# Performance work log

Hardware: AMD Instinct MI355X
Metric: run time of the kernel (lower is better)

## Reference

```python
import jax, jax.numpy as jnp
import numpy as np

ALPHA = 0.12
BETA = 0.88
OMEGA = 6.0
PHI_BASE = 0.0
B, T, D = 4, 4096, 2048


def setup_inputs() -> dict:
    key = jax.random.key(0)
    k1, = jax.random.split(key, 1)
    x = jax.random.normal(k1, (B, T, D), dtype=jnp.float32)
    gate = jnp.asarray(-2.0, dtype=jnp.float32)          # nn.Parameter gate_init
    input_scale = jnp.asarray(4.0, dtype=jnp.float32)     # nn.Parameter init 4.0
    mem_state = jnp.zeros((1, 1, D), dtype=jnp.float32)   # persistent buffer
    return {"x": x, "gate": gate, "input_scale": input_scale,
            "mem_state": mem_state, "step_idx": 0}


def reference(x, gate, input_scale, mem_state, step_idx):
    Bn, Tn, Dn = x.shape
    dtype = x.dtype
    # EMA recurrence: m_t = beta * m_{t-1} + alpha * input_scale * x_t
    u = (ALPHA * input_scale) * x                         # [B,T,D]
    m0 = jnp.broadcast_to(mem_state[:, 0, :], (Bn, Dn))   # [B,D]

    def step(m, u_t):
        m = BETA * m + u_t
        return m, m

    _, ms = jax.lax.scan(step, m0, jnp.swapaxes(u, 0, 1))  # [T,B,D]
    ms = jnp.swapaxes(ms, 0, 1)                            # [B,T,D]

    # log-periodic phase rotation per step (scalar angle per t)
    t_glob = jnp.arange(1, Tn + 1, dtype=dtype) + jnp.asarray(step_idx, dtype)
    theta = (OMEGA * jnp.log1p(t_glob) + PHI_BASE) % (2.0 * jnp.pi)  # [T]
    c = jnp.cos(theta)[None, :, None]
    s = jnp.sin(theta)[None, :, None]
    half = Dn // 2  # D even -> no tail
    a = ms[..., :half]
    b = ms[..., half:2 * half]
    m_rot = jnp.concatenate([a * c - b * s, a * s + b * c], axis=-1)  # [B,T,D]

    # residual gated output: y = x + sigmoid(gate) * m_seq
    return x + jax.nn.sigmoid(gate) * m_rot
```

## Files before the change

### kernel.cpp

```cpp
#include <hip/hip_runtime.h>
#include <math.h>

#define ALPHA 0.12f
#define BETA  0.88f
#define OMEGA 6.0f
#define TWO_PI 6.28318530717958647692f

constexpr int Bn   = 4;
constexpr int Tn   = 4096;
constexpr int Dn   = 2048;
constexpr int HALF = Dn / 2;
constexpr int L    = 16;
constexpr int NC   = Tn / L;

typedef float fx4 __attribute__((ext_vector_type(4)));

constexpr float beta_pow(int n) {
    float r = 1.0f;
    for (int i = 0; i < n; ++i) r *= BETA;
    return r;
}
constexpr float BETA_L = beta_pow(L);

__global__ __launch_bounds__(256) void k_chunksum(
        const float* __restrict__ x,
        const float* __restrict__ input_scale,
        float* __restrict__ S) {
    int gid = blockIdx.x * blockDim.x + threadIdx.x;
    int d4 = gid & (Dn / 4 - 1);
    int c  = (gid >> 9) & (NC - 1);
    int b  = gid >> 17;
    const float sc = ALPHA * (*input_scale);

    const fx4* xp = (const fx4*)(x + ((size_t)b * Tn + (size_t)c * L) * Dn) + d4;
    fx4 m = (fx4)(0.0f);
#pragma unroll
    for (int i = 0; i < L; ++i) {
        fx4 v = xp[(size_t)i * (Dn / 4)];
        m = BETA * m + sc * v;
    }
    ((fx4*)S)[gid] = m;
}

__global__ __launch_bounds__(256) void k_final(
        const float* __restrict__ x,
        const float* __restrict__ gate,
        const float* __restrict__ input_scale,
        const float* __restrict__ S,
        const float* __restrict__ mem_state,
        const int*   __restrict__ step_idx,
        float* __restrict__ out) {
    int p4 = threadIdx.x;
    int c  = blockIdx.x & (NC - 1);
    int b  = blockIdx.x >> 8;

    const float sc  = ALPHA * (*input_scale);
    const float sig = 1.0f / (1.0f + expf(-(*gate)));

    __shared__ float cs[L];
    __shared__ float ss[L];
    if (threadIdx.x < L) {
        int t = c * L + threadIdx.x;
        float tg = (float)(t + 1 + *step_idx);
        float theta = fmodf(OMEGA * log1pf(tg), TWO_PI);
        cs[threadIdx.x] = cosf(theta);
        ss[threadIdx.x] = sinf(theta);
    }

    fx4 ma = ((const fx4*)mem_state)[p4];
    fx4 mb = ((const fx4*)mem_state)[p4 + HALF / 4];
    const fx4* Sa = (const fx4*)(S + (size_t)b * NC * Dn) + p4;
    const fx4* Sb = Sa + HALF / 4;
#pragma unroll 8
    for (int j = 0; j < c; ++j) {
        ma = BETA_L * ma + Sa[(size_t)j * (Dn / 4)];
        mb = BETA_L * mb + Sb[(size_t)j * (Dn / 4)];
    }
    __syncthreads();

    size_t base = ((size_t)b * Tn + (size_t)c * L) * Dn;
    const fx4* xa = (const fx4*)(x + base) + p4;
    const fx4* xb = (const fx4*)(x + base + HALF) + p4;
    fx4* oa = (fx4*)(out + base) + p4;
    fx4* ob = (fx4*)(out + base + HALF) + p4;

#pragma unroll 8
    for (int i = 0; i < L; ++i) {
        fx4 va = xa[(size_t)i * (Dn / 4)];
        fx4 vb = xb[(size_t)i * (Dn / 4)];
        ma = BETA * ma + sc * va;
        mb = BETA * mb + sc * vb;
        float cth = cs[i];
        float sth = ss[i];
        fx4 ra = va + sig * (ma * cth - mb * sth);
        fx4 rb = vb + sig * (ma * sth + mb * cth);
        __builtin_nontemporal_store(ra, &oa[(size_t)i * (Dn / 4)]);
        __builtin_nontemporal_store(rb, &ob[(size_t)i * (Dn / 4)]);
    }
}

extern "C" void kernel_launch(void* const* d_in, const int* in_sizes, int n_in,
                              void* d_out, int out_size, void* d_ws, size_t ws_size,
                              hipStream_t stream) {
    const float* x           = (const float*)d_in[0];
    const float* gate        = (const float*)d_in[1];
    const float* input_scale = (const float*)d_in[2];
    const float* mem_state   = (const float*)d_in[3];
    const int*   step_idx    = (const int*)d_in[4];
    float* out = (float*)d_out;

    float* S = (float*)d_ws;

    k_chunksum<<<(Bn * NC * Dn / 4) / 256, 256, 0, stream>>>(x, input_scale, S);
    k_final<<<Bn * NC, 256, 0, stream>>>(x, gate, input_scale, S,
                                         mem_state, step_idx, out);
}
```

Baseline: 310.5 us.

## Replace per-block prefix recomputation with a separate sequential carry-propagation kernel

```diff
diff --git a/kernel.cpp b/kernel.cpp
--- a/kernel.cpp
+++ b/kernel.cpp
@@ -10,8 +10,8 @@
 constexpr int Tn   = 4096;
 constexpr int Dn   = 2048;
 constexpr int HALF = Dn / 2;
-constexpr int L    = 16;
-constexpr int NC   = Tn / L;
+constexpr int G    = 16;
+constexpr int NQ   = Tn / G;
 
 typedef float fx4 __attribute__((ext_vector_type(4)));
 
@@ -20,72 +20,80 @@
     for (int i = 0; i < n; ++i) r *= BETA;
     return r;
 }
-constexpr float BETA_L = beta_pow(L);
+constexpr float BETA_G = beta_pow(G);
 
-__global__ __launch_bounds__(256) void k_chunksum(
+__global__ __launch_bounds__(256) void k_sub(
         const float* __restrict__ x,
         const float* __restrict__ input_scale,
         float* __restrict__ S) {
     int gid = blockIdx.x * blockDim.x + threadIdx.x;
     int d4 = gid & (Dn / 4 - 1);
-    int c  = (gid >> 9) & (NC - 1);
+    int q  = (gid >> 9) & (NQ - 1);
     int b  = gid >> 17;
     const float sc = ALPHA * (*input_scale);
 
-    const fx4* xp = (const fx4*)(x + ((size_t)b * Tn + (size_t)c * L) * Dn) + d4;
+    const fx4* xp = (const fx4*)(x + ((size_t)b * Tn + (size_t)q * G) * Dn) + d4;
     fx4 m = (fx4)(0.0f);
 #pragma unroll
-    for (int i = 0; i < L; ++i) {
+    for (int i = 0; i < G; ++i) {
         fx4 v = xp[(size_t)i * (Dn / 4)];
         m = BETA * m + sc * v;
     }
     ((fx4*)S)[gid] = m;
 }
 
+__global__ __launch_bounds__(256) void k_carry(
+        float* __restrict__ S,
+        const float* __restrict__ mem_state) {
+    int gid = blockIdx.x * blockDim.x + threadIdx.x;
+    int d4 = gid & (Dn / 4 - 1);
+    int b  = gid >> 9;
+
+    fx4 m = ((const fx4*)mem_state)[d4];
+    fx4* Sp = (fx4*)S + (size_t)b * NQ * (Dn / 4) + d4;
+    for (int q = 0; q < NQ; ++q) {
+        fx4 s = Sp[(size_t)q * (Dn / 4)];
+        Sp[(size_t)q * (Dn / 4)] = m;
+        m = BETA_G * m + s;
+    }
+}
 __global__ __launch_bounds__(256) void k_final(
         const float* __restrict__ x,
         const float* __restrict__ gate,
         const float* __restrict__ input_scale,
         const float* __restrict__ S,
-        const float* __restrict__ mem_state,
         const int*   __restrict__ step_idx,
         float* __restrict__ out) {
     int p4 = threadIdx.x;
-    int c  = blockIdx.x & (NC - 1);
+    int q  = blockIdx.x & (NQ - 1);
     int b  = blockIdx.x >> 8;
 
     const float sc  = ALPHA * (*input_scale);
     const float sig = 1.0f / (1.0f + expf(-(*gate)));
 
-    __shared__ float cs[L];
-    __shared__ float ss[L];
-    if (threadIdx.x < L) {
-        int t = c * L + threadIdx.x;
+    __shared__ float cs[G];
+    __shared__ float ss[G];
+    if (threadIdx.x < G) {
+        int t = q * G + threadIdx.x;
         float tg = (float)(t + 1 + *step_idx);
         float theta = fmodf(OMEGA * log1pf(tg), TWO_PI);
         cs[threadIdx.x] = cosf(theta);
         ss[threadIdx.x] = sinf(theta);
     }
 
-    fx4 ma = ((const fx4*)mem_state)[p4];
-    fx4 mb = ((const fx4*)mem_state)[p4 + HALF / 4];
-    const fx4* Sa = (const fx4*)(S + (size_t)b * NC * Dn) + p4;
-    const fx4* Sb = Sa + HALF / 4;
-#pragma unroll 8
-    for (int j = 0; j < c; ++j) {
-        ma = BETA_L * ma + Sa[(size_t)j * (Dn / 4)];
-        mb = BETA_L * mb + Sb[(size_t)j * (Dn / 4)];
-    }
+    const fx4* Fp = (const fx4*)S + (size_t)(b * NQ + q) * (Dn / 4);
+    fx4 ma = Fp[p4];
+    fx4 mb = Fp[HALF / 4 + p4];
     __syncthreads();
 
-    size_t base = ((size_t)b * Tn + (size_t)c * L) * Dn;
+    size_t base = ((size_t)b * Tn + (size_t)q * G) * Dn;
     const fx4* xa = (const fx4*)(x + base) + p4;
     const fx4* xb = (const fx4*)(x + base + HALF) + p4;
     fx4* oa = (fx4*)(out + base) + p4;
     fx4* ob = (fx4*)(out + base + HALF) + p4;
 
-#pragma unroll 8
-    for (int i = 0; i < L; ++i) {
+#pragma unroll
+    for (int i = 0; i < G; ++i) {
         fx4 va = xa[(size_t)i * (Dn / 4)];
         fx4 vb = xb[(size_t)i * (Dn / 4)];
         ma = BETA * ma + sc * va;
@@ -111,7 +119,8 @@
 
     float* S = (float*)d_ws;
 
-    k_chunksum<<<(Bn * NC * Dn / 4) / 256, 256, 0, stream>>>(x, input_scale, S);
-    k_final<<<Bn * NC, 256, 0, stream>>>(x, gate, input_scale, S,
-                                         mem_state, step_idx, out);
+    k_sub<<<(Bn * NQ * Dn / 4) / 256, 256, 0, stream>>>(x, input_scale, S);
+    k_carry<<<(Bn * Dn / 4) / 256, 256, 0, stream>>>(S, mem_state);
+    k_final<<<Bn * NQ, 256, 0, stream>>>(x, gate, input_scale, S,
+                                         step_idx, out);
 }
```

Measured after the change: 282.0 us. 9.2% less time.
